# Optimization experiments

Hardware: AMD Instinct MI355X
Metric: run time of the kernel (lower is better)

Reference implementation:

```python
import jax, jax.numpy as jnp
import numpy as np

B, M, H = 8, 2048, 1024


def setup_inputs() -> dict:
    key = jax.random.key(0)
    k0, k1, k2, k3, k4 = jax.random.split(key, 5)
    return {
        "query": jax.random.normal(k0, (B, M, H), dtype=jnp.float32),
        "key": jax.random.normal(k1, (B, M, H), dtype=jnp.float32),
        "span": jax.random.uniform(k2, (B, M, 2), dtype=jnp.float32),
        "value": jax.random.normal(k3, (B, M, H), dtype=jnp.float32),
        "key_pe": jax.random.normal(k4, (1, H, M), dtype=jnp.float32),
    }


def reference(query, key, span, value, key_pe):
    # Faithful to the source's returned value:
    #   attn_cont (span-gathered version) is overwritten by the dense q @ k^T,
    #   and the scaled/softmaxed `attn` (content + positional) is computed but
    #   NEVER used for the output. The module returns attn_cont @ value with
    #   no scaling and no softmax. span / key_pe do not affect the output.
    attn_cont = jnp.einsum('bmh,bnh->bmn', query, key)  # [B, M, M]
    out = jnp.matmul(attn_cont, value)                   # [B, M, H]
    return out
```

## Files before the change

kernel.cpp:

```cpp
#include <hip/hip_runtime.h>
#include <hip/hip_bf16.h>

typedef __attribute__((ext_vector_type(4))) float f32x4;
typedef __attribute__((ext_vector_type(8))) short bf16x8;
typedef __attribute__((ext_vector_type(8))) unsigned short u16x8;
typedef __attribute__((ext_vector_type(2))) unsigned int u32x2;
typedef unsigned short u16;
typedef unsigned int u32;


__device__ __forceinline__ u16 f2bf(float f) {
  union { float f; unsigned int u; } v;
  v.f = f;
  unsigned int r = (v.u + 0x7fffu + ((v.u >> 16) & 1u)) >> 16;
  return (u16)r;
}

__device__ __forceinline__ u32 pk2(float a, float b) {
  u32 r;
  asm("v_cvt_pk_bf16_f32 %0, %1, %2" : "=v"(r) : "v"(a), "v"(b));
  return r;
}

__device__ __forceinline__ void async16(const void* g, const void* l) {
  __builtin_amdgcn_global_load_lds(
      (const __attribute__((address_space(1))) unsigned int*)(unsigned long)g,
      (__attribute__((address_space(3))) unsigned int*)(unsigned int)(unsigned long)l,
      16, 0, 0);
}

__device__ __forceinline__ void bar() {
  asm volatile("" ::: "memory");
  __builtin_amdgcn_s_barrier();
  asm volatile("" ::: "memory");
}

#define WAIT_VM0() asm volatile("s_waitcnt vmcnt(0)" ::: "memory")


__global__ __launch_bounds__(256) void cvt_plain(const float* __restrict__ in,
                                                 u16* __restrict__ out, int n4) {
  int stride = gridDim.x * blockDim.x;
  for (int i = blockIdx.x * blockDim.x + threadIdx.x; i < n4; i += stride) {
    f32x4 v = *(const f32x4*)(in + (long)i * 4);
    ushort4 o;
    o.x = f2bf(v.x); o.y = f2bf(v.y); o.z = f2bf(v.z); o.w = f2bf(v.w);
    *(ushort4*)(out + (long)i * 4) = o;
  }
}


__global__ __launch_bounds__(256) void cvt_kv(const float* __restrict__ Kin,
                                              const float* __restrict__ Vin,
                                              u16* __restrict__ Kt,
                                              u16* __restrict__ Vt) {
  __shared__ char tile[16384];

  const int z = blockIdx.z;
  const int bsel = z >> 1;
  const float* in = (z & 1) ? Kin : Vin;
  u16* out = (z & 1) ? Kt : Vt;
  const long bo = (long)bsel * 2048 * 1024;
  const int r0 = blockIdx.y * 128;
  const int c0 = blockIdx.x * 64;

  const int t = threadIdx.x;
  const int c4 = (t & 15) * 4;
  const int n4b = (t >> 4) * 4;

  f32x4 v[2][4];
#pragma unroll
  for (int i = 0; i < 2; ++i)
#pragma unroll
    for (int r = 0; r < 3 + 1; ++r)
      v[i][r] = *(const f32x4*)(in + bo + (long)(r0 + i * 64 + n4b + r) * 1024 +
                                c0 + c4);

#pragma unroll
  for (int i = 0; i < 2; ++i) {
    const int n4 = i * 64 + n4b;
    const int grp = n4 >> 3;
    const int sub = (n4 & 4) * 2;
#pragma unroll
    for (int q = 0; q < 4; ++q) {
      const int c = c4 + q;
      u32x2 w;
      w.x = pk2(v[i][0][q], v[i][1][q]);
      w.y = pk2(v[i][2][q], v[i][3][q]);
      *(u32x2*)(tile + c * 256 + ((grp ^ (c & 15)) << 4) + sub) = w;
    }
  }
  __syncthreads();

  const int g = t & 15;
#pragma unroll
  for (int p = 0; p < 4; ++p) {
    const int c = (t >> 4) + p * 16;
    u16x8 u = *(const u16x8*)(tile + c * 256 + ((g ^ (c & 15)) << 4));
    *(u16x8*)(out + bo + (long)(c0 + c) * 2048 + r0 + g * 8) = u;
  }
}

template <bool BF16OUT>
__global__ __launch_bounds__(512, 2) void gemm_nt(const u16* __restrict__ A,
                                                  const u16* __restrict__ Bt,
                                                  void* __restrict__ Cv,
                                                  int K, int NT, int nTN,
                                                  long sA, long sB, long sC) {
  __shared__ u16 As[2][256][64];
  __shared__ u16 Bs[2][128][64];

  const int bid = blockIdx.x;
  const int b = bid & 7;
  const int tile = bid >> 3;
  const int bn0 = (tile % nTN) * 128;
  const int bm0 = (tile / nTN) * 256;

  const int tid = threadIdx.x;
  const int lane = tid & 63;
  const int wave = tid >> 6;
  const int wr = wave >> 2;
  const int wc = wave & 3;
  const int l16 = lane & 15;
  const int kh = lane >> 4;

  const char* Ab = (const char*)(A + (long)b * sA);
  const char* Bb = (const char*)(Bt + (long)b * sB);

  const int rowbytes = K * 2;
  int aoff[4], boff[2];
#pragma unroll
  for (int i = 0; i < 4; ++i) {
    int u = tid + i * 512;
    int row = u >> 3, sl = (u & 7) ^ (row & 7);
    aoff[i] = (bm0 + row) * rowbytes + sl * 16;
  }
#pragma unroll
  for (int i = 0; i < 2; ++i) {
    int u = tid + i * 512;
    int row = u >> 3, sl = (u & 7) ^ (row & 7);
    boff[i] = (bn0 + row) * rowbytes + sl * 16;
  }

#define STG_A(buf)                                                          \
  {                                                                         \
    _Pragma("unroll") for (int i_ = 0; i_ < 4; ++i_) {                      \
      async16(Ab + aoff[i_], (char*)&As[buf][0][0] + (tid + i_ * 512) * 16);\
      aoff[i_] += 128;                                                      \
    }                                                                       \
  }
#define STG_B(buf)                                                          \
  {                                                                         \
    _Pragma("unroll") for (int i_ = 0; i_ < 2; ++i_) {                      \
      async16(Bb + boff[i_], (char*)&Bs[buf][0][0] + (tid + i_ * 512) * 16);\
      boff[i_] += 128;                                                      \
    }                                                                       \
  }

  int offA[2][4][2];
#pragma unroll
  for (int q = 0; q < 2; ++q)
#pragma unroll
    for (int f = 0; f < 4; ++f) {
      int r = q * 128 + wr * 64 + f * 16 + l16;
#pragma unroll
      for (int ks = 0; ks < 2; ++ks)
        offA[q][f][ks] = r * 64 + (((ks * 4 + kh) ^ (l16 & 7)) * 8);
    }
  int offB[2][2];
#pragma unroll
  for (int fn = 0; fn < 2; ++fn) {
    int r = fn * 64 + wc * 16 + l16;
#pragma unroll
    for (int ks = 0; ks < 2; ++ks)
      offB[fn][ks] = r * 64 + (((ks * 4 + kh) ^ (l16 & 7)) * 8);
  }

  f32x4 acc[8][2] = {};
  bf16x8 ar[4][2], br[2][2];

  STG_A(0); STG_B(0);
  WAIT_VM0();
  bar();

  for (int t = 0; t < NT; ++t) {
    const int cur = t & 1, nxt = cur ^ 1;
    const bool g = (t + 1 < NT);
    const u16* Abuf = &As[cur][0][0];
    const u16* Bbuf = &Bs[cur][0][0];

#pragma unroll
    for (int f = 0; f < 4; ++f)
#pragma unroll
      for (int ks = 0; ks < 2; ++ks)
        ar[f][ks] = *(const bf16x8*)(Abuf + offA[0][f][ks]);
#pragma unroll
    for (int fn = 0; fn < 2; ++fn)
#pragma unroll
      for (int ks = 0; ks < 2; ++ks)
        br[fn][ks] = *(const bf16x8*)(Bbuf + offB[fn][ks]);

    if (g) { STG_A(nxt); STG_B(nxt); }

    __builtin_amdgcn_s_setprio(1);
#pragma unroll
    for (int f = 0; f < 4; ++f)
#pragma unroll
      for (int n = 0; n < 2; ++n)
#pragma unroll
        for (int ks = 0; ks < 2; ++ks)
          acc[f][n] = __builtin_amdgcn_mfma_f32_16x16x32_bf16(
              ar[f][ks], br[n][ks], acc[f][n], 0, 0, 0);
    __builtin_amdgcn_s_setprio(0);

#pragma unroll
    for (int f = 0; f < 4; ++f)
#pragma unroll
      for (int ks = 0; ks < 2; ++ks)
        ar[f][ks] = *(const bf16x8*)(Abuf + offA[1][f][ks]);

    __builtin_amdgcn_s_setprio(1);
#pragma unroll
    for (int f = 0; f < 4; ++f)
#pragma unroll
      for (int n = 0; n < 2; ++n)
#pragma unroll
        for (int ks = 0; ks < 2; ++ks)
          acc[4 + f][n] = __builtin_amdgcn_mfma_f32_16x16x32_bf16(
              ar[f][ks], br[n][ks], acc[4 + f][n], 0, 0, 0);
    __builtin_amdgcn_s_setprio(0);

    if (g) WAIT_VM0();
    bar();
  }
#undef STG_A
#undef STG_B

  u16*   Cb = (u16*)Cv + (long)b * sC;
  float* Cf = (float*)Cv + (long)b * sC;
#pragma unroll
  for (int fm = 0; fm < 8; ++fm) {
    const int gm = bm0 + (fm >> 2) * 128 + wr * 64 + (fm & 3) * 16 + kh * 4;
#pragma unroll
    for (int fn = 0; fn < 2; ++fn) {
      const int gn = bn0 + fn * 64 + wc * 16 + l16;
#pragma unroll
      for (int r = 0; r < 4; ++r) {
        if (BF16OUT) Cb[(long)(gm + r) * 1024 + gn] = f2bf(acc[fm][fn][r]);
        else         Cf[(long)(gm + r) * 1024 + gn] = acc[fm][fn][r];
      }
    }
  }
}


extern "C" void kernel_launch(void* const* d_in, const int* in_sizes, int n_in,
                              void* d_out, int out_size, void* d_ws, size_t ws_size,
                              hipStream_t stream) {
  const float* Q  = (const float*)d_in[0];
  const float* Kf = (const float*)d_in[1];
  const float* V  = (const float*)d_in[3];
  float* out = (float*)d_out;

  char* ws = (char*)d_ws;
  u16* Vt = (u16*)(ws);
  u16* Kt = (u16*)(ws + (size_t)32 * 1024 * 1024);
  u16* Pt = (u16*)(ws + (size_t)64 * 1024 * 1024);
  u16* Qb = (u16*)(ws + (size_t)80 * 1024 * 1024);

  cvt_kv<<<dim3(16, 16, 16), 256, 0, stream>>>(Kf, V, Kt, Vt);
  cvt_plain<<<4096, 256, 0, stream>>>(Q, Qb, 8 * 2048 * 1024 / 4);

  gemm_nt<true><<<256, 512, 0, stream>>>(
      Vt, Kt, (void*)Pt, 2048, 32, 8,
      (long)1024 * 2048, (long)1024 * 2048, (long)1024 * 1024);

  gemm_nt<false><<<512, 512, 0, stream>>>(
      Qb, Pt, (void*)out, 1024, 16, 8,
      (long)2048 * 1024, (long)1024 * 1024, (long)2048 * 1024);
}
```

Measured before the change: 135.4 us.

## Store transposed K/V and intermediate P in K-blocked 64-wide panels

The transposed bf16 K and V, and the intermediate P = V^T K, are now stored in panel-major layout: contiguous 64-element-wide column blocks with 128-byte rows. The GEMM kernel takes separate row-stride and k-step parameters, so each k-step tile load reads one contiguous panel instead of striding across long rows. The convert kernel is reshaped to write full panel rows with a new LDS swizzle, and the first GEMM's epilogue writes P directly in panel form. The aim is better global-load and cache locality for the async tile staging, at the cost of more index arithmetic and a layout coupling that every stage must agree on.

```diff
diff --git a/kernel.cpp b/kernel.cpp
--- a/kernel.cpp
+++ b/kernel.cpp
@@ -54,50 +54,47 @@
                                               const float* __restrict__ Vin,
                                               u16* __restrict__ Kt,
                                               u16* __restrict__ Vt) {
-  __shared__ char tile[16384];
+  __shared__ char tile[32768];
 
   const int z = blockIdx.z;
   const int bsel = z >> 1;
   const float* in = (z & 1) ? Kin : Vin;
   u16* out = (z & 1) ? Kt : Vt;
   const long bo = (long)bsel * 2048 * 1024;
-  const int r0 = blockIdx.y * 128;
-  const int c0 = blockIdx.x * 64;
+  const int n0 = blockIdx.y * 64;
+  const int c0 = blockIdx.x * 256;
 
   const int t = threadIdx.x;
-  const int c4 = (t & 15) * 4;
-  const int n4b = (t >> 4) * 4;
-
-  f32x4 v[2][4];
-#pragma unroll
-  for (int i = 0; i < 2; ++i)
-#pragma unroll
-    for (int r = 0; r < 3 + 1; ++r)
-      v[i][r] = *(const f32x4*)(in + bo + (long)(r0 + i * 64 + n4b + r) * 1024 +
-                                c0 + c4);
-
-#pragma unroll
-  for (int i = 0; i < 2; ++i) {
-    const int n4 = i * 64 + n4b;
-    const int grp = n4 >> 3;
-    const int sub = (n4 & 4) * 2;
+  const int c4 = (t & 63) * 4;
+  const int nr = t >> 6;
+
+#pragma unroll
+  for (int g = 0; g < 4; ++g) {
+    const int n4 = g * 16 + nr * 4;
+    f32x4 v[4];
+#pragma unroll
+    for (int r = 0; r < 4; ++r)
+      v[r] = *(const f32x4*)(in + bo + (long)(n0 + n4 + r) * 1024 + c0 + c4);
+    const int s = n4 >> 2;
 #pragma unroll
     for (int q = 0; q < 4; ++q) {
       const int c = c4 + q;
+      const int ssw = ((c >> 2) & 7) << 1;
       u32x2 w;
-      w.x = pk2(v[i][0][q], v[i][1][q]);
-      w.y = pk2(v[i][2][q], v[i][3][q]);
-      *(u32x2*)(tile + c * 256 + ((grp ^ (c & 15)) << 4) + sub) = w;
+      w.x = pk2(v[0][q], v[1][q]);
+      w.y = pk2(v[2][q], v[3][q]);
+      *(u32x2*)(tile + c * 128 + ((s ^ ssw) << 3)) = w;
     }
   }
   __syncthreads();
 
-  const int g = t & 15;
-#pragma unroll
-  for (int p = 0; p < 4; ++p) {
-    const int c = (t >> 4) + p * 16;
-    u16x8 u = *(const u16x8*)(tile + c * 256 + ((g ^ (c & 15)) << 4));
-    *(u16x8*)(out + bo + (long)(c0 + c) * 2048 + r0 + g * 8) = u;
+  const long ob = bo + (long)blockIdx.y * 65536 + (long)c0 * 64;
+#pragma unroll
+  for (int p = 0; p < 8; ++p) {
+    const int c = (t >> 3) + p * 32;
+    const int gp = (t & 7) ^ ((c >> 2) & 7);
+    u16x8 u = *(const u16x8*)(tile + c * 128 + (gp << 4));
+    *(u16x8*)(out + ob + p * 2048 + t * 8) = u;
   }
 }
 
@@ -105,8 +102,10 @@
 __global__ __launch_bounds__(512, 2) void gemm_nt(const u16* __restrict__ A,
                                                   const u16* __restrict__ Bt,
                                                   void* __restrict__ Cv,
-                                                  int K, int NT, int nTN,
-                                                  long sA, long sB, long sC) {
+                                                  int NT, int nTN,
+                                                  long sA, long sB, long sC,
+                                                  int aRow, int aStep,
+                                                  int bRow, int bStep) {
   __shared__ u16 As[2][256][64];
   __shared__ u16 Bs[2][128][64];
 
@@ -127,33 +126,32 @@
   const char* Ab = (const char*)(A + (long)b * sA);
   const char* Bb = (const char*)(Bt + (long)b * sB);
 
-  const int rowbytes = K * 2;
   int aoff[4], boff[2];
 #pragma unroll
   for (int i = 0; i < 4; ++i) {
     int u = tid + i * 512;
     int row = u >> 3, sl = (u & 7) ^ (row & 7);
-    aoff[i] = (bm0 + row) * rowbytes + sl * 16;
+    aoff[i] = (bm0 + row) * aRow + sl * 16;
   }
 #pragma unroll
   for (int i = 0; i < 2; ++i) {
     int u = tid + i * 512;
     int row = u >> 3, sl = (u & 7) ^ (row & 7);
-    boff[i] = (bn0 + row) * rowbytes + sl * 16;
+    boff[i] = (bn0 + row) * bRow + sl * 16;
   }
 
 #define STG_A(buf)                                                          \
   {                                                                         \
     _Pragma("unroll") for (int i_ = 0; i_ < 4; ++i_) {                      \
       async16(Ab + aoff[i_], (char*)&As[buf][0][0] + (tid + i_ * 512) * 16);\
-      aoff[i_] += 128;                                                      \
+      aoff[i_] += aStep;                                                    \
     }                                                                       \
   }
 #define STG_B(buf)                                                          \
   {                                                                         \
     _Pragma("unroll") for (int i_ = 0; i_ < 2; ++i_) {                      \
       async16(Bb + boff[i_], (char*)&Bs[buf][0][0] + (tid + i_ * 512) * 16);\
-      boff[i_] += 128;                                                      \
+      boff[i_] += bStep;                                                    \
     }                                                                       \
   }
 
@@ -243,11 +241,15 @@
     const int gm = bm0 + (fm >> 2) * 128 + wr * 64 + (fm & 3) * 16 + kh * 4;
 #pragma unroll
     for (int fn = 0; fn < 2; ++fn) {
-      const int gn = bn0 + fn * 64 + wc * 16 + l16;
 #pragma unroll
       for (int r = 0; r < 4; ++r) {
-        if (BF16OUT) Cb[(long)(gm + r) * 1024 + gn] = f2bf(acc[fm][fn][r]);
-        else         Cf[(long)(gm + r) * 1024 + gn] = acc[fm][fn][r];
+        if (BF16OUT) {
+          Cb[(long)((bn0 >> 6) + fn) * 65536 + (long)(gm + r) * 64 +
+             wc * 16 + l16] = f2bf(acc[fm][fn][r]);
+        } else {
+          const int gn = bn0 + fn * 64 + wc * 16 + l16;
+          Cf[(long)(gm + r) * 1024 + gn] = acc[fm][fn][r];
+        }
       }
     }
   }
@@ -268,14 +270,16 @@
   u16* Pt = (u16*)(ws + (size_t)64 * 1024 * 1024);
   u16* Qb = (u16*)(ws + (size_t)80 * 1024 * 1024);
 
-  cvt_kv<<<dim3(16, 16, 16), 256, 0, stream>>>(Kf, V, Kt, Vt);
+  cvt_kv<<<dim3(4, 32, 16), 256, 0, stream>>>(Kf, V, Kt, Vt);
   cvt_plain<<<4096, 256, 0, stream>>>(Q, Qb, 8 * 2048 * 1024 / 4);
 
   gemm_nt<true><<<256, 512, 0, stream>>>(
-      Vt, Kt, (void*)Pt, 2048, 32, 8,
-      (long)1024 * 2048, (long)1024 * 2048, (long)1024 * 1024);
+      Vt, Kt, (void*)Pt, 32, 8,
+      (long)1024 * 2048, (long)1024 * 2048, (long)1024 * 1024,
+      128, 131072, 128, 131072);
 
   gemm_nt<false><<<512, 512, 0, stream>>>(
-      Qb, Pt, (void*)out, 1024, 16, 8,
-      (long)2048 * 1024, (long)1024 * 1024, (long)2048 * 1024);
-}
+      Qb, Pt, (void*)out, 16, 8,
+      (long)2048 * 1024, (long)1024 * 1024, (long)2048 * 1024,
+      2048, 128, 128, 131072);
+}
```

After: 141.3 us. 1.04x slower.
